# Performance work log

Hardware: AMD Instinct MI355X
Metric: run time of the kernel (lower is better)

## Reference

```python
import jax, jax.numpy as jnp
import numpy as np

N_NODES = 100000
N_EDGES = 1600000
IN_CH, HID_CH, OUT_CH = 128, 128, 64


def _sage_conv(x, src, dst, deg_inv, W_l, b_l, W_r):
    # PyG SAGEConv (mean aggr): out = lin_l(mean_{j in N(i)} x_j) + lin_r(x_i)
    msg = x[src]                                   # [E, C_in] gather
    agg = jax.ops.segment_sum(msg, dst, num_segments=N_NODES)  # [N, C_in]
    agg = agg * deg_inv[:, None]
    return agg @ W_l.T + b_l + x @ W_r.T


def setup_inputs() -> dict:
    key = jax.random.key(0)
    ks = jax.random.split(key, 10)
    x = jax.random.normal(ks[0], (N_NODES, IN_CH), dtype=jnp.float32)
    edge_attr = jax.random.normal(ks[1], (N_EDGES, 4), dtype=jnp.float32)
    edge_index = jax.random.randint(ks[2], (2, N_EDGES), 0, N_NODES, dtype=jnp.int32)
    dims = [(IN_CH, HID_CH), (HID_CH, HID_CH), (HID_CH, OUT_CH)]
    params = {}
    for i, (cin, cout) in enumerate(dims):
        s = 1.0 / np.sqrt(cin)
        params[f"W_l{i}"] = jax.random.uniform(ks[3 + 2 * i], (cout, cin), minval=-s, maxval=s, dtype=jnp.float32)
        params[f"b_l{i}"] = jnp.zeros((cout,), dtype=jnp.float32)
        params[f"W_r{i}"] = jax.random.uniform(ks[4 + 2 * i], (cout, cin), minval=-s, maxval=s, dtype=jnp.float32)
    return {"x": x, "edge_attr": edge_attr, "edge_index": edge_index, **params}


def reference(x, edge_attr, edge_index,
              W_l0, b_l0, W_r0,
              W_l1, b_l1, W_r1,
              W_l2, b_l2, W_r2):
    src, dst = edge_index[0], edge_index[1]
    deg = jax.ops.segment_sum(jnp.ones((N_EDGES,), jnp.float32), dst, num_segments=N_NODES)
    deg_inv = 1.0 / jnp.maximum(deg, 1.0)
    layers = [(W_l0, b_l0, W_r0), (W_l1, b_l1, W_r1), (W_l2, b_l2, W_r2)]
    h = x
    for i, (Wl, bl, Wr) in enumerate(layers):
        h = _sage_conv(h, src, dst, deg_inv, Wl, bl, Wr)
        if i != len(layers) - 1:
            h = jax.nn.relu(h)
            # dropout is identity in eval mode (training=False)
    return h
```

## Files before the change

### kernel.cpp

```cpp
#include <hip/hip_runtime.h>
#include <cstdint>

#define N_NODES 100000
#define N_EDGES 1600000

constexpr int NCB = 196;
constexpr int HB  = 391;

typedef __attribute__((ext_vector_type(8))) short short8;
typedef __attribute__((ext_vector_type(4))) float f32x4;

__device__ inline uint32_t fbits(float f) { union { float f; uint32_t u; } c; c.f = f; return c.u; }
__device__ inline float bfloat(uint32_t u) { union { uint32_t u; float f; } c; c.u = u; return c.f; }

__device__ inline void bsplit(float a, short& hi, short& lo) {
    uint32_t h = fbits(a) & 0xFFFF0000u;
    float fl = a - bfloat(h);
    hi = (short)(h >> 16);
    lo = (short)(fbits(fl) >> 16);
}

__device__ inline ushort f2bf(float f) {
    uint32_t u = fbits(f);
    return (ushort)((u + 0x7FFFu + ((u >> 16) & 1u)) >> 16);
}


__global__ __launch_bounds__(256)
void hist_kernel(const int* __restrict__ dst, int* __restrict__ H) {
    __shared__ int h[NCB];
    for (int i = threadIdx.x; i < NCB; i += 256) h[i] = 0;
    __syncthreads();
    int e0 = blockIdx.x * 4096;
    #pragma unroll
    for (int it = 0; it < 16; ++it) {
        int e = e0 + it * 256 + threadIdx.x;
        if (e < N_EDGES) atomicAdd(&h[dst[e] >> 9], 1);
    }
    __syncthreads();
    for (int i = threadIdx.x; i < NCB; i += 256) H[blockIdx.x * NCB + i] = h[i];
}

__global__ __launch_bounds__(256)
void scanbase_kernel(int* __restrict__ H, int* __restrict__ boff) {
    __shared__ int tot[NCB];
    __shared__ int base[NCB + 1];
    int j = threadIdx.x;
    if (j < NCB) {
        int s = 0;
        for (int b = 0; b < HB; ++b) s += H[b * NCB + j];
        tot[j] = s;
    }
    __syncthreads();
    if (j == 0) {
        int run = 0;
        for (int k = 0; k < NCB; ++k) { base[k] = run; run += tot[k]; }
        base[NCB] = run;
    }
    __syncthreads();
    if (j <= NCB) boff[j] = base[j];
    if (j < NCB) {
        int run = base[j];
        for (int b = 0; b < HB; ++b) {
            int v = H[b * NCB + j];
            H[b * NCB + j] = run;
            run += v;
        }
    }
}

__global__ __launch_bounds__(256)
void scatter_kernel(const int* __restrict__ src, const int* __restrict__ dst,
                    const int* __restrict__ H, uint32_t* __restrict__ ebuf) {
    __shared__ int cur[NCB];
    for (int i = threadIdx.x; i < NCB; i += 256) cur[i] = H[blockIdx.x * NCB + i];
    __syncthreads();
    int e0 = blockIdx.x * 4096;
    #pragma unroll
    for (int it = 0; it < 16; ++it) {
        int e = e0 + it * 256 + threadIdx.x;
        if (e < N_EDGES) {
            int d = dst[e];
            int p = atomicAdd(&cur[d >> 9], 1);
            ebuf[p] = ((uint32_t)src[e] << 9) | (uint32_t)(d & 511);
        }
    }
}


__global__ __launch_bounds__(256)
void bucket_csr(const uint32_t* __restrict__ ebuf, const int* __restrict__ boff,
                int* __restrict__ off, float* __restrict__ dinv,
                int* __restrict__ ssrc) {
    __shared__ int deg[512];
    __shared__ int cur[512];
    __shared__ int wsum[4];
    int t = threadIdx.x, lane = t & 63, w = t >> 6;
    int j = blockIdx.x;
    int base = boff[j], end = boff[j + 1];
    int node0 = j << 9;

    deg[t] = 0; deg[t + 256] = 0;
    __syncthreads();

    for (int p = base + t; p < end; p += 256)
        atomicAdd(&deg[ebuf[p] & 511u], 1);
    __syncthreads();

    int d0 = deg[2 * t], d1 = deg[2 * t + 1];
    int s = d0 + d1;
    int incl = s;
    #pragma unroll
    for (int d = 1; d < 64; d <<= 1) {
        int u = __shfl_up(incl, d);
        if (lane >= d) incl += u;
    }
    if (lane == 63) wsum[w] = incl;
    __syncthreads();
    if (t < 4) {
        int v = wsum[t];
        int iv = v;
        #pragma unroll
        for (int d = 1; d < 4; d <<= 1) {
            int u = __shfl_up(iv, d, 4);
            if (t >= d) iv += u;
        }
        wsum[t] = iv - v;
    }
    __syncthreads();
    int ebase = wsum[w] + (incl - s);
    cur[2 * t] = ebase;
    cur[2 * t + 1] = ebase + d0;
    int n0 = node0 + 2 * t, n1 = n0 + 1;
    if (n0 < N_NODES) {
        off[n0] = base + ebase;
        dinv[n0] = 1.0f / (float)max(d0, 1);
    }
    if (n1 < N_NODES) {
        off[n1] = base + ebase + d0;
        dinv[n1] = 1.0f / (float)max(d1, 1);
    }
    if (j == 0 && t == 0) off[N_NODES] = N_EDGES;
    __syncthreads();

    for (int p = base + t; p < end; p += 256) {
        uint32_t ent = ebuf[p];
        int pos = atomicAdd(&cur[ent & 511u], 1);
        ssrc[base + pos] = (int)(ent >> 9);
    }
}


__global__ void wfrag_kernel(const float* __restrict__ W1, const float* __restrict__ W2,
                             int C1, int NCT, int ntask,
                             short* __restrict__ fhi, short* __restrict__ flo) {
    int tau = blockIdx.x * 256 + threadIdx.x;
    if (tau >= ntask) return;
    int lane = tau & 63;
    int ct = (tau >> 6) % NCT;
    int ks = (tau >> 6) / NCT;
    int col = ct * 16 + (lane & 15);
    int k = ks * 32 + (lane >> 4) * 8;
    const float* p = (col < C1) ? &W1[(size_t)col * 128 + k]
                                : &W2[(size_t)(col - C1) * 128 + k];
    short8 h8, l8;
    #pragma unroll
    for (int j = 0; j < 8; ++j) {
        short h, l;
        bsplit(p[j], h, l);
        h8[j] = h; l8[j] = l;
    }
    *reinterpret_cast<short8*>(&fhi[(size_t)tau * 8]) = h8;
    *reinterpret_cast<short8*>(&flo[(size_t)tau * 8]) = l8;
}


template<int C1, int C2>
__global__ __launch_bounds__(256)
void gemm_mfma(const float* __restrict__ H, const short* __restrict__ Wfhi,
               const short* __restrict__ Wflo, const float* __restrict__ bias2,
               ushort* __restrict__ out1, float* __restrict__ out2) {
    constexpr int COUT = C1 + C2;
    constexpr int CT = COUT / 64;
    constexpr int NCT = COUT / 16;
    __shared__ short Ahi[64 * 128];
    __shared__ short Alo[64 * 128];
    int t = threadIdx.x;
    int l = t & 63, w = t >> 6;
    int lr = l & 15, kg = l >> 4;
    int r0 = blockIdx.x * 64;
    int c_base = w * (COUT / 4);
    const bool is1 = (c_base < C1);

    #pragma unroll
    for (int it = 0; it < 4; ++it) {
        int lin = t + it * 256;
        int row = lin >> 4, ch = lin & 15;
        float av[8];
        if (r0 + row < N_NODES) {
            const float* p = &H[(size_t)(r0 + row) * 128 + ch * 8];
            float4 v0 = *reinterpret_cast<const float4*>(p);
            float4 v1 = *reinterpret_cast<const float4*>(p + 4);
            av[0] = v0.x; av[1] = v0.y; av[2] = v0.z; av[3] = v0.w;
            av[4] = v1.x; av[5] = v1.y; av[6] = v1.z; av[7] = v1.w;
        } else {
            #pragma unroll
            for (int j = 0; j < 8; ++j) av[j] = 0.f;
        }
        short8 h8, l8;
        #pragma unroll
        for (int j = 0; j < 8; ++j) {
            short h, lo2;
            bsplit(av[j], h, lo2);
            h8[j] = h; l8[j] = lo2;
        }
        int off = row * 128 + ((ch ^ (row & 7)) << 3);
        *reinterpret_cast<short8*>(&Ahi[off]) = h8;
        *reinterpret_cast<short8*>(&Alo[off]) = l8;
    }
    __syncthreads();

    f32x4 acc[4][CT];
    #pragma unroll
    for (int m = 0; m < 4; ++m)
        #pragma unroll
        for (int c = 0; c < CT; ++c)
            acc[m][c] = (f32x4){0.f, 0.f, 0.f, 0.f};

    #pragma unroll
    for (int ks = 0; ks < 4; ++ks) {
        int ch = ks * 4 + kg;
        short8 ahi[4], alo[4];
        #pragma unroll
        for (int m = 0; m < 4; ++m) {
            int row = m * 16 + lr;
            int off = row * 128 + ((ch ^ (row & 7)) << 3);
            ahi[m] = *reinterpret_cast<const short8*>(&Ahi[off]);
            alo[m] = *reinterpret_cast<const short8*>(&Alo[off]);
        }
        short8 bhi[CT], blo[CT];
        #pragma unroll
        for (int c = 0; c < CT; ++c) {
            int ctg = w * CT + c;
            size_t fo = ((size_t)(ks * NCT + ctg) * 64 + l) * 8;
            bhi[c] = *reinterpret_cast<const short8*>(&Wfhi[fo]);
            blo[c] = *reinterpret_cast<const short8*>(&Wflo[fo]);
        }
        #pragma unroll
        for (int m = 0; m < 4; ++m)
            #pragma unroll
            for (int c = 0; c < CT; ++c) {
                acc[m][c] = __builtin_amdgcn_mfma_f32_16x16x32_bf16(ahi[m], bhi[c], acc[m][c], 0, 0, 0);
                acc[m][c] = __builtin_amdgcn_mfma_f32_16x16x32_bf16(ahi[m], blo[c], acc[m][c], 0, 0, 0);
                acc[m][c] = __builtin_amdgcn_mfma_f32_16x16x32_bf16(alo[m], bhi[c], acc[m][c], 0, 0, 0);
            }
    }

    if (is1) {
        #pragma unroll
        for (int c = 0; c < CT; ++c) {
            int col = c_base + c * 16 + lr;
            #pragma unroll
            for (int m = 0; m < 4; ++m)
                #pragma unroll
                for (int r = 0; r < 4; ++r) {
                    int row = r0 + m * 16 + kg * 4 + r;
                    if (row < N_NODES)
                        out1[(size_t)row * C1 + col] = f2bf(acc[m][c][r]);
                }
        }
    } else {
        #pragma unroll
        for (int c = 0; c < CT; ++c) {
            int col = c_base - C1 + c * 16 + lr;
            float bb = bias2[col];
            #pragma unroll
            for (int m = 0; m < 4; ++m)
                #pragma unroll
                for (int r = 0; r < 4; ++r) {
                    int row = r0 + m * 16 + kg * 4 + r;
                    if (row < N_NODES)
                        out2[(size_t)row * C2 + col] = acc[m][c][r] + bb;
                }
        }
    }
}


template<int C, bool RELU>
__global__ __launch_bounds__(256)
void agg_wave(const ushort* __restrict__ Y, const int* __restrict__ off,
              const int* __restrict__ ssrc, const float* __restrict__ dinv,
              float* __restrict__ out) {
    constexpr int NCH = C / 8;
    constexpr int ESL = 64 / NCH;
    int t = threadIdx.x, l = t & 63;
    int i = blockIdx.x * 4 + (t >> 6);
    int chunk = l & (NCH - 1);
    int eslot = l / NCH;
    int p0 = off[i], p1 = off[i + 1];

    float acc[8] = {0.f, 0.f, 0.f, 0.f, 0.f, 0.f, 0.f, 0.f};
    for (int p = p0; p < p1; p += 2 * ESL) {
        #pragma unroll
        for (int u = 0; u < 2; ++u) {
            int q = p + u * ESL + eslot;
            if (q < p1) {
                int s = ssrc[q];
                uint4 v = *reinterpret_cast<const uint4*>(&Y[(size_t)s * C + chunk * 8]);
                uint32_t wd[4] = {v.x, v.y, v.z, v.w};
                #pragma unroll
                for (int j = 0; j < 4; ++j) {
                    acc[2 * j]     += bfloat(wd[j] << 16);
                    acc[2 * j + 1] += bfloat(wd[j] & 0xFFFF0000u);
                }
            }
        }
    }
    #pragma unroll
    for (int d = NCH; d < 64; d <<= 1)
        #pragma unroll
        for (int j = 0; j < 8; ++j)
            acc[j] += __shfl_xor(acc[j], d);

    if (eslot == 0) {
        float di = dinv[i];
        float* op = &out[(size_t)i * C + chunk * 8];
        float4 z0 = *reinterpret_cast<const float4*>(op);
        float4 z1 = *reinterpret_cast<const float4*>(op + 4);
        float zz[8] = {z0.x, z0.y, z0.z, z0.w, z1.x, z1.y, z1.z, z1.w};
        float r[8];
        #pragma unroll
        for (int j = 0; j < 8; ++j) {
            r[j] = acc[j] * di + zz[j];
            if (RELU) r[j] = fmaxf(r[j], 0.f);
        }
        *reinterpret_cast<float4*>(op)     = make_float4(r[0], r[1], r[2], r[3]);
        *reinterpret_cast<float4*>(op + 4) = make_float4(r[4], r[5], r[6], r[7]);
    }
}


extern "C" void kernel_launch(void* const* d_in, const int* in_sizes, int n_in,
                              void* d_out, int out_size, void* d_ws, size_t ws_size,
                              hipStream_t stream) {
    const float* x   = (const float*)d_in[0];
    const int*   ei  = (const int*)d_in[2];
    const float* Wl0 = (const float*)d_in[3];
    const float* bl0 = (const float*)d_in[4];
    const float* Wr0 = (const float*)d_in[5];
    const float* Wl1 = (const float*)d_in[6];
    const float* bl1 = (const float*)d_in[7];
    const float* Wr1 = (const float*)d_in[8];
    const float* Wl2 = (const float*)d_in[9];
    const float* bl2 = (const float*)d_in[10];
    const float* Wr2 = (const float*)d_in[11];
    float* out = (float*)d_out;

    char* ws = (char*)d_ws;
    int*      H    = (int*)(ws + 0);
    int*      boff = (int*)(ws + (size_t)(384 << 10));
    int*      off  = (int*)(ws + (size_t)(512 << 10));
    float*    dinv = (float*)(ws + (size_t)(960 << 10));
    uint32_t* ebuf = (uint32_t*)(ws + (size_t)(1400 << 10));
    int*      ssrc = (int*)(ws + (size_t)(1400 << 10) + (size_t)(7 << 20));
    short* w0hi = (short*)(ws + (size_t)(16 << 20));
    short* w0lo = w0hi + 32768;
    short* w1hi = w0lo + 32768;
    short* w1lo = w1hi + 32768;
    short* w2hi = w1lo + 32768;
    short* w2lo = w2hi + 16384;
    ushort* Ybf = (ushort*)(ws + (size_t)(18 << 20));
    float* bufB = (float*)(ws + (size_t)(46 << 20));

    const int* srcp = ei;
    const int* dstp = ei + N_EDGES;

    hist_kernel<<<HB, 256, 0, stream>>>(dstp, H);
    scanbase_kernel<<<1, 256, 0, stream>>>(H, boff);
    scatter_kernel<<<HB, 256, 0, stream>>>(srcp, dstp, H, ebuf);
    bucket_csr<<<NCB, 256, 0, stream>>>(ebuf, boff, off, dinv, ssrc);

    wfrag_kernel<<<16, 256, 0, stream>>>(Wl0, Wr0, 128, 16, 4096, w0hi, w0lo);
    wfrag_kernel<<<16, 256, 0, stream>>>(Wl1, Wr1, 128, 16, 4096, w1hi, w1lo);
    wfrag_kernel<<<8, 256, 0, stream>>>(Wl2, Wr2, 64, 8, 2048, w2hi, w2lo);

    int ggrid = (N_NODES + 63) / 64;
    int wgrid = (N_NODES + 3) / 4;

    gemm_mfma<128, 128><<<ggrid, 256, 0, stream>>>(x, w0hi, w0lo, bl0, Ybf, bufB);
    agg_wave<128, true><<<wgrid, 256, 0, stream>>>(Ybf, off, ssrc, dinv, bufB);

    gemm_mfma<128, 128><<<ggrid, 256, 0, stream>>>(bufB, w1hi, w1lo, bl1, Ybf, bufB);
    agg_wave<128, true><<<wgrid, 256, 0, stream>>>(Ybf, off, ssrc, dinv, bufB);

    gemm_mfma<64, 64><<<ggrid, 256, 0, stream>>>(bufB, w2hi, w2lo, bl2, Ybf, out);
    agg_wave<64, false><<<wgrid, 256, 0, stream>>>(Ybf, off, ssrc, dinv, out);
}
```

Measured before the change: 390.5 us.

## Store intermediate activations and root terms in bf16 to cut memory traffic

```diff
diff --git a/kernel.cpp b/kernel.cpp
--- a/kernel.cpp
+++ b/kernel.cpp
@@ -24,6 +24,9 @@
     uint32_t u = fbits(f);
     return (ushort)((u + 0x7FFFu + ((u >> 16) & 1u)) >> 16);
 }
+
+__device__ inline void zstore(ushort* p, float v) { *p = f2bf(v); }
+__device__ inline void zstore(float* p, float v) { *p = v; }
 
 
 __global__ __launch_bounds__(256)
@@ -177,9 +180,9 @@
 
 template<int C1, int C2>
 __global__ __launch_bounds__(256)
-void gemm_mfma(const float* __restrict__ H, const short* __restrict__ Wfhi,
-               const short* __restrict__ Wflo, const float* __restrict__ bias2,
-               ushort* __restrict__ out1, float* __restrict__ out2) {
+void gemm_f32(const float* __restrict__ H, const short* __restrict__ Wfhi,
+              const short* __restrict__ Wflo, const float* __restrict__ bias2,
+              ushort* __restrict__ out1, ushort* __restrict__ out2) {
     constexpr int COUT = C1 + C2;
     constexpr int CT = COUT / 64;
     constexpr int NCT = COUT / 16;
@@ -256,42 +259,113 @@
             }
     }
 
-    if (is1) {
+    #pragma unroll
+    for (int c = 0; c < CT; ++c) {
+        int colg = c_base + c * 16 + lr;
+        int col = is1 ? colg : colg - C1;
+        float bb = is1 ? 0.f : bias2[col];
+        ushort* dst = is1 ? out1 : out2;
+        int cw = is1 ? C1 : C2;
+        #pragma unroll
+        for (int m = 0; m < 4; ++m)
+            #pragma unroll
+            for (int r = 0; r < 4; ++r) {
+                int row = r0 + m * 16 + kg * 4 + r;
+                if (row < N_NODES)
+                    dst[(size_t)row * cw + col] = f2bf(acc[m][c][r] + bb);
+            }
+    }
+}
+
+
+template<int C1, int C2, typename ZT>
+__global__ __launch_bounds__(256)
+void gemm_bf16(const ushort* __restrict__ H, const short* __restrict__ Wfhi,
+               const short* __restrict__ Wflo, const float* __restrict__ bias2,
+               ushort* __restrict__ out1, ZT* __restrict__ out2) {
+    constexpr int COUT = C1 + C2;
+    constexpr int CT = COUT / 64;
+    constexpr int NCT = COUT / 16;
+    __shared__ short A[64 * 128];
+    int t = threadIdx.x;
+    int l = t & 63, w = t >> 6;
+    int lr = l & 15, kg = l >> 4;
+    int r0 = blockIdx.x * 64;
+    int c_base = w * (COUT / 4);
+    const bool is1 = (c_base < C1);
+
+    #pragma unroll
+    for (int it = 0; it < 4; ++it) {
+        int lin = t + it * 256;
+        int row = lin >> 4, ch = lin & 15;
+        short8 v = (short8){0, 0, 0, 0, 0, 0, 0, 0};
+        if (r0 + row < N_NODES)
+            v = *reinterpret_cast<const short8*>(&H[(size_t)(r0 + row) * 128 + ch * 8]);
+        int off = row * 128 + ((ch ^ (row & 7)) << 3);
+        *reinterpret_cast<short8*>(&A[off]) = v;
+    }
+    __syncthreads();
+
+    f32x4 acc[4][CT];
+    #pragma unroll
+    for (int m = 0; m < 4; ++m)
+        #pragma unroll
+        for (int c = 0; c < CT; ++c)
+            acc[m][c] = (f32x4){0.f, 0.f, 0.f, 0.f};
+
+    #pragma unroll
+    for (int ks = 0; ks < 4; ++ks) {
+        int ch = ks * 4 + kg;
+        short8 a[4];
+        #pragma unroll
+        for (int m = 0; m < 4; ++m) {
+            int row = m * 16 + lr;
+            int off = row * 128 + ((ch ^ (row & 7)) << 3);
+            a[m] = *reinterpret_cast<const short8*>(&A[off]);
+        }
+        short8 bhi[CT], blo[CT];
         #pragma unroll
         for (int c = 0; c < CT; ++c) {
-            int col = c_base + c * 16 + lr;
+            int ctg = w * CT + c;
+            size_t fo = ((size_t)(ks * NCT + ctg) * 64 + l) * 8;
+            bhi[c] = *reinterpret_cast<const short8*>(&Wfhi[fo]);
+            blo[c] = *reinterpret_cast<const short8*>(&Wflo[fo]);
+        }
+        #pragma unroll
+        for (int m = 0; m < 4; ++m)
             #pragma unroll
-            for (int m = 0; m < 4; ++m)
-                #pragma unroll
-                for (int r = 0; r < 4; ++r) {
-                    int row = r0 + m * 16 + kg * 4 + r;
-                    if (row < N_NODES)
-                        out1[(size_t)row * C1 + col] = f2bf(acc[m][c][r]);
+            for (int c = 0; c < CT; ++c) {
+                acc[m][c] = __builtin_amdgcn_mfma_f32_16x16x32_bf16(a[m], bhi[c], acc[m][c], 0, 0, 0);
+                acc[m][c] = __builtin_amdgcn_mfma_f32_16x16x32_bf16(a[m], blo[c], acc[m][c], 0, 0, 0);
+            }
+    }
+
+    #pragma unroll
+    for (int c = 0; c < CT; ++c) {
+        int colg = c_base + c * 16 + lr;
+        #pragma unroll
+        for (int m = 0; m < 4; ++m)
+            #pragma unroll
+            for (int r = 0; r < 4; ++r) {
+                int row = r0 + m * 16 + kg * 4 + r;
+                if (row < N_NODES) {
+                    if (is1) {
+                        out1[(size_t)row * C1 + colg] = f2bf(acc[m][c][r]);
+                    } else {
+                        int col = colg - C1;
+                        zstore(&out2[(size_t)row * C2 + col], acc[m][c][r] + bias2[col]);
+                    }
                 }
-        }
-    } else {
-        #pragma unroll
-        for (int c = 0; c < CT; ++c) {
-            int col = c_base - C1 + c * 16 + lr;
-            float bb = bias2[col];
-            #pragma unroll
-            for (int m = 0; m < 4; ++m)
-                #pragma unroll
-                for (int r = 0; r < 4; ++r) {
-                    int row = r0 + m * 16 + kg * 4 + r;
-                    if (row < N_NODES)
-                        out2[(size_t)row * C2 + col] = acc[m][c][r] + bb;
-                }
-        }
-    }
-}
-
-
-template<int C, bool RELU>
-__global__ __launch_bounds__(256)
-void agg_wave(const ushort* __restrict__ Y, const int* __restrict__ off,
-              const int* __restrict__ ssrc, const float* __restrict__ dinv,
-              float* __restrict__ out) {
+            }
+    }
+}
+
+
+template<int C, bool FINAL>
+__global__ __launch_bounds__(256)
+void agg_wave(const ushort* __restrict__ Y, const void* __restrict__ Zv,
+              const int* __restrict__ off, const int* __restrict__ ssrc,
+              const float* __restrict__ dinv, void* __restrict__ outv) {
     constexpr int NCH = C / 8;
     constexpr int ESL = 64 / NCH;
     int t = threadIdx.x, l = t & 63;
@@ -301,9 +375,9 @@
     int p0 = off[i], p1 = off[i + 1];
 
     float acc[8] = {0.f, 0.f, 0.f, 0.f, 0.f, 0.f, 0.f, 0.f};
-    for (int p = p0; p < p1; p += 2 * ESL) {
-        #pragma unroll
-        for (int u = 0; u < 2; ++u) {
+    for (int p = p0; p < p1; p += 4 * ESL) {
+        #pragma unroll
+        for (int u = 0; u < 4; ++u) {
             int q = p + u * ESL + eslot;
             if (q < p1) {
                 int s = ssrc[q];
@@ -325,18 +399,44 @@
 
     if (eslot == 0) {
         float di = dinv[i];
-        float* op = &out[(size_t)i * C + chunk * 8];
-        float4 z0 = *reinterpret_cast<const float4*>(op);
-        float4 z1 = *reinterpret_cast<const float4*>(op + 4);
-        float zz[8] = {z0.x, z0.y, z0.z, z0.w, z1.x, z1.y, z1.z, z1.w};
+        float zz[8];
+        if (FINAL) {
+            const float* Z = (const float*)Zv;
+            const float* zp = &Z[(size_t)i * C + chunk * 8];
+            float4 z0 = *reinterpret_cast<const float4*>(zp);
+            float4 z1 = *reinterpret_cast<const float4*>(zp + 4);
+            zz[0] = z0.x; zz[1] = z0.y; zz[2] = z0.z; zz[3] = z0.w;
+            zz[4] = z1.x; zz[5] = z1.y; zz[6] = z1.z; zz[7] = z1.w;
+        } else {
+            const ushort* Z = (const ushort*)Zv;
+            uint4 zv = *reinterpret_cast<const uint4*>(&Z[(size_t)i * C + chunk * 8]);
+            uint32_t wd[4] = {zv.x, zv.y, zv.z, zv.w};
+            #pragma unroll
+            for (int j = 0; j < 4; ++j) {
+                zz[2 * j]     = bfloat(wd[j] << 16);
+                zz[2 * j + 1] = bfloat(wd[j] & 0xFFFF0000u);
+            }
+        }
         float r[8];
         #pragma unroll
         for (int j = 0; j < 8; ++j) {
             r[j] = acc[j] * di + zz[j];
-            if (RELU) r[j] = fmaxf(r[j], 0.f);
-        }
-        *reinterpret_cast<float4*>(op)     = make_float4(r[0], r[1], r[2], r[3]);
-        *reinterpret_cast<float4*>(op + 4) = make_float4(r[4], r[5], r[6], r[7]);
+            if (!FINAL) r[j] = fmaxf(r[j], 0.f);
+        }
+        if (FINAL) {
+            float* O = (float*)outv;
+            float* op = &O[(size_t)i * C + chunk * 8];
+            *reinterpret_cast<float4*>(op)     = make_float4(r[0], r[1], r[2], r[3]);
+            *reinterpret_cast<float4*>(op + 4) = make_float4(r[4], r[5], r[6], r[7]);
+        } else {
+            ushort* O = (ushort*)outv;
+            uint4 o;
+            o.x = (uint32_t)f2bf(r[0]) | ((uint32_t)f2bf(r[1]) << 16);
+            o.y = (uint32_t)f2bf(r[2]) | ((uint32_t)f2bf(r[3]) << 16);
+            o.z = (uint32_t)f2bf(r[4]) | ((uint32_t)f2bf(r[5]) << 16);
+            o.w = (uint32_t)f2bf(r[6]) | ((uint32_t)f2bf(r[7]) << 16);
+            *reinterpret_cast<uint4*>(&O[(size_t)i * C + chunk * 8]) = o;
+        }
     }
 }
 
@@ -371,7 +471,8 @@
     short* w2hi = w1lo + 32768;
     short* w2lo = w2hi + 16384;
     ushort* Ybf = (ushort*)(ws + (size_t)(18 << 20));
-    float* bufB = (float*)(ws + (size_t)(46 << 20));
+    ushort* Zbf = (ushort*)(ws + (size_t)(44 << 20));
+    ushort* Hbf = (ushort*)(ws + (size_t)(70 << 20));
 
     const int* srcp = ei;
     const int* dstp = ei + N_EDGES;
@@ -388,12 +489,12 @@
     int ggrid = (N_NODES + 63) / 64;
     int wgrid = (N_NODES + 3) / 4;
 
-    gemm_mfma<128, 128><<<ggrid, 256, 0, stream>>>(x, w0hi, w0lo, bl0, Ybf, bufB);
-    agg_wave<128, true><<<wgrid, 256, 0, stream>>>(Ybf, off, ssrc, dinv, bufB);
-
-    gemm_mfma<128, 128><<<ggrid, 256, 0, stream>>>(bufB, w1hi, w1lo, bl1, Ybf, bufB);
-    agg_wave<128, true><<<wgrid, 256, 0, stream>>>(Ybf, off, ssrc, dinv, bufB);
-
-    gemm_mfma<64, 64><<<ggrid, 256, 0, stream>>>(bufB, w2hi, w2lo, bl2, Ybf, out);
-    agg_wave<64, false><<<wgrid, 256, 0, stream>>>(Ybf, off, ssrc, dinv, out);
-}
+    gemm_f32<128, 128><<<ggrid, 256, 0, stream>>>(x, w0hi, w0lo, bl0, Ybf, Zbf);
+    agg_wave<128, false><<<wgrid, 256, 0, stream>>>(Ybf, Zbf, off, ssrc, dinv, Hbf);
+
+    gemm_bf16<128, 128, ushort><<<ggrid, 256, 0, stream>>>(Hbf, w1hi, w1lo, bl1, Ybf, Zbf);
+    agg_wave<128, false><<<wgrid, 256, 0, stream>>>(Ybf, Zbf, off, ssrc, dinv, Hbf);
+
+    gemm_bf16<64, 64, float><<<ggrid, 256, 0, stream>>>(Hbf, w2hi, w2lo, bl2, Ybf, (float*)Zbf);
+    agg_wave<64, true><<<wgrid, 256, 0, stream>>>(Ybf, (const void*)Zbf, off, ssrc, dinv, out);
+}
```

New measurement: 374.7 us. 1.04x faster.
